# Kernel tuning notes

Measured on AMD Instinct MI355X. Metric: run time of the kernel, lower is better.

## Reference

```python
import jax, jax.numpy as jnp
import numpy as np

B, IN, K, T = 2048, 512, 16, 96
H = K // 2            # LSTM hidden per direction
L = IN - K + 1        # number of sliding patches


def setup_inputs() -> dict:
    key = jax.random.key(0)
    ks = jax.random.split(key, 16)
    def n(k, shape, s=0.1):
        return jax.random.normal(k, shape, dtype=jnp.float32) * s
    return {
        "x": jax.random.normal(ks[0], (B, IN), dtype=jnp.float32),
        "pe": n(ks[1], (L, K)),                                   # learnable positional encoding
        "W_seg": n(ks[2], (K, K)), "b_seg": jnp.zeros((K,), jnp.float32),
        "g_bn": jnp.ones((L,), jnp.float32), "b_bn": jnp.zeros((L,), jnp.float32),
        "Wih_f0": n(ks[3], (4 * H, K)),  "Whh_f0": n(ks[4], (4 * H, H)),
        "Wih_b0": n(ks[5], (4 * H, K)),  "Whh_b0": n(ks[6], (4 * H, H)),
        "Wih_f1": n(ks[7], (4 * H, 2 * H)), "Whh_f1": n(ks[8], (4 * H, H)),
        "Wih_b1": n(ks[9], (4 * H, 2 * H)), "Whh_b1": n(ks[10], (4 * H, H)),
        "g_ln": jnp.ones((K,), jnp.float32), "b_ln": jnp.zeros((K,), jnp.float32),
        "W1": n(ks[11], (512, K)), "b1": jnp.zeros((512,), jnp.float32),
        "W2": n(ks[12], (1, 512)), "b2": jnp.zeros((1,), jnp.float32),
    }


def _cell(h, c, x_t, Wih, Whh):
    # PyTorch LSTM cell, no bias; gate order i,f,g,o
    g = x_t @ Wih.T + h @ Whh.T
    i, f, gg, o = jnp.split(g, 4, axis=-1)
    c_new = jax.nn.sigmoid(f) * c + jax.nn.sigmoid(i) * jnp.tanh(gg)
    h_new = jax.nn.sigmoid(o) * jnp.tanh(c_new)
    return h_new, c_new


def _run_dir(xs, Wih, Whh, reverse):
    # xs: [B, L, D]; one LSTM direction via lax.scan over time
    z = jnp.zeros((xs.shape[0], Whh.shape[1]), xs.dtype)
    def step(carry, x_t):
        h, c = carry
        h, c = _cell(h, c, x_t, Wih, Whh)
        return (h, c), h
    (hT, cT), ys = jax.lax.scan(step, (z, z), jnp.swapaxes(xs, 0, 1), reverse=reverse)
    return jnp.swapaxes(ys, 0, 1), hT, cT


def _ln(z, g, b, eps=1e-5):
    m = z.mean(-1, keepdims=True)
    v = ((z - m) ** 2).mean(-1, keepdims=True)
    return (z - m) * jax.lax.rsqrt(v + eps) * g + b


def reference(x, pe, W_seg, b_seg, g_bn, b_bn, Wih_f0, Whh_f0, Wih_b0, Whh_b0,
              Wih_f1, Whh_f1, Wih_b1, Whh_b1, g_ln, b_ln, W1, b1, W2, b2):
    # SegmentationBlock: unfold -> +PE -> Linear -> GELU -> BatchNorm1d(L)
    idx = jnp.arange(L)[:, None] + jnp.arange(K)[None, :]
    p = x[:, idx] + pe                                     # [B, L, K]
    p = jax.nn.gelu(p @ W_seg.T + b_seg, approximate=False)
    mu = p.mean(axis=(0, 2), keepdims=True)                # BN over channel dim L (batch stats)
    var = p.var(axis=(0, 2), keepdims=True)
    xe = (p - mu) * jax.lax.rsqrt(var + 1e-5) * g_bn[None, :, None] + b_bn[None, :, None]
    # 2-layer bidirectional LSTM encoder
    of0, hf0, cf0 = _run_dir(xe, Wih_f0, Whh_f0, False)
    ob0, hb0, cb0 = _run_dir(xe, Wih_b0, Whh_b0, True)
    o0 = jnp.concatenate([of0, ob0], -1)                   # [B, L, 2H=K]
    of1, hf1, cf1 = _run_dir(o0, Wih_f1, Whh_f1, False)
    ob1, hb1, cb1 = _run_dir(o0, Wih_b1, Whh_b1, True)
    out = jnp.concatenate([of1, ob1], -1)                  # [B, L, K]
    out = _ln(out, g_ln, b_ln) + xe
    def dec(z):  # FCBlock, dropout off (eval)
        h = jax.nn.gelu(z @ W1.T + b1, approximate=False)
        return h @ W2.T + b2                               # [B, 1]
    fb = out[:, -1, :]                                     # [B, K]
    def step(carry, _):
        hf0, cf0, hb0, cb0, hf1, cf1, hb1, cb1, fb = carry
        hf0, cf0 = _cell(hf0, cf0, fb, Wih_f0, Whh_f0)
        hb0, cb0 = _cell(hb0, cb0, fb, Wih_b0, Whh_b0)
        m0 = jnp.concatenate([hf0, hb0], -1)
        hf1, cf1 = _cell(hf1, cf1, m0, Wih_f1, Whh_f1)
        hb1, cb1 = _cell(hb1, cb1, m0, Wih_b1, Whh_b1)
        o = jnp.concatenate([hf1, hb1], -1)                # [B, K]
        y = dec(_ln(o, g_ln, b_ln))[:, 0]                  # [B]
        return (hf0, cf0, hb0, cb0, hf1, cf1, hb1, cb1, o), y
    init = (hf0, cf0, hb0, cb0, hf1, cf1, hb1, cb1, fb)
    _, ys = jax.lax.scan(step, init, None, length=T)
    return jnp.swapaxes(ys, 0, 1)                          # [B, T]
```

## Files before the change

kernel.cpp:

```cpp
#include <hip/hip_runtime.h>
#include <math.h>

#define NB 2048
#define NIN 512
#define NK 16
#define NL 497
#define NT 96
#define NREP 32

__device__ __forceinline__ float gelu_exact(float x) {
    return 0.5f * x * (1.0f + erff(x * 0.70710678118654752440f));
}
__device__ __forceinline__ float gate_act(float acc, bool isG) {
    float mm = isG ? 2.0f : 1.0f;
    float e  = __expf(-mm * acc);
    float s  = 1.0f / (1.0f + e);
    return isG ? 2.0f * s - 1.0f : s;
}
__device__ __forceinline__ float tanh_safe(float x) {
    float t = __expf(-2.0f * fabsf(x));
    float r = 1.0f - 2.0f * t / (1.0f + t);
    return copysignf(r, x);
}
__device__ __forceinline__ void load16(const float* __restrict__ ptr, float* dst) {
    const float4* rp = (const float4*)ptr;
    float4 a = rp[0], b = rp[1], c = rp[2], d = rp[3];
    dst[0]=a.x; dst[1]=a.y; dst[2]=a.z;  dst[3]=a.w;
    dst[4]=b.x; dst[5]=b.y; dst[6]=b.z;  dst[7]=b.w;
    dst[8]=c.x; dst[9]=c.y; dst[10]=c.z; dst[11]=c.w;
    dst[12]=d.x;dst[13]=d.y;dst[14]=d.z; dst[15]=d.w;
}

template<int PRAW>
__global__ __launch_bounds__(256) void k_seg(
    const float* __restrict__ x, const float* __restrict__ pe,
    const float* __restrict__ Wseg, const float* __restrict__ bseg,
    const float* __restrict__ Wf0, const float* __restrict__ Wb0,
    float* __restrict__ praw, float* __restrict__ pfull,
    float* __restrict__ p_last, float* __restrict__ bn)
{
    __shared__ float xs[NIN];
    __shared__ float wsg[NK * NK];
    __shared__ float bs[NK];
    __shared__ float wf[32 * 16];
    __shared__ float wb[32 * 16];
    const int tid = threadIdx.x;
    const int b = blockIdx.x;
    float* bnr = bn + (size_t)(b & (NREP - 1)) * 1024;
    for (int i = tid; i < NIN; i += 256) xs[i] = x[(size_t)b * NIN + i];
    if (tid < NK * NK) wsg[tid] = Wseg[tid];
    if (tid < NK) bs[tid] = bseg[tid];
    if constexpr (PRAW) {
        for (int i = tid; i < 512; i += 256) { wf[i] = Wf0[i]; wb[i] = Wb0[i]; }
    }
    __syncthreads();

    for (int l = tid; l < NL; l += 256) {
        float u[NK];
        load16(pe + l * NK, u);
        #pragma unroll
        for (int k = 0; k < NK; k++) u[k] += xs[l + k];
        float p16[NK];
        float s = 0.f, s2 = 0.f;
        #pragma unroll
        for (int k = 0; k < NK; k++) {
            float acc = bs[k];
            #pragma unroll
            for (int kp = 0; kp < NK; kp++) acc += u[kp] * wsg[k * NK + kp];
            float gv = gelu_exact(acc);
            p16[k] = gv; s += gv; s2 += gv * gv;
        }
        atomicAdd(&bnr[l], s);
        atomicAdd(&bnr[512 + l], s2);

        if constexpr (PRAW) {
            float* pf = praw + ((size_t)b * NL + l) * 64;
            float* pb = praw + ((size_t)b * NL + (NL - 1 - l)) * 64 + 32;
            #pragma unroll 2
            for (int gq = 0; gq < 8; gq++) {
                float4 o;
                float* op = (float*)&o;
                #pragma unroll
                for (int q = 0; q < 4; q++) {
                    const float* wr = &wf[(gq * 4 + q) * 16];
                    float a0 = 0.f;
                    #pragma unroll
                    for (int k = 0; k < 16; k++) a0 += p16[k] * wr[k];
                    op[q] = a0;
                }
                ((float4*)pf)[gq] = o;
            }
            #pragma unroll 2
            for (int gq = 0; gq < 8; gq++) {
                float4 o;
                float* op = (float*)&o;
                #pragma unroll
                for (int q = 0; q < 4; q++) {
                    const float* wr = &wb[(gq * 4 + q) * 16];
                    float a0 = 0.f;
                    #pragma unroll
                    for (int k = 0; k < 16; k++) a0 += p16[k] * wr[k];
                    op[q] = a0;
                }
                ((float4*)pb)[gq] = o;
            }
        } else {
            float4* pr = (float4*)(pfull + ((size_t)b * NL + l) * NK);
            pr[0] = make_float4(p16[0], p16[1], p16[2], p16[3]);
            pr[1] = make_float4(p16[4], p16[5], p16[6], p16[7]);
            pr[2] = make_float4(p16[8], p16[9], p16[10], p16[11]);
            pr[3] = make_float4(p16[12], p16[13], p16[14], p16[15]);
        }
        if (l == NL - 1) {
            float4* pl = (float4*)(p_last + (size_t)b * NK);
            pl[0] = make_float4(p16[0], p16[1], p16[2], p16[3]);
            pl[1] = make_float4(p16[4], p16[5], p16[6], p16[7]);
            pl[2] = make_float4(p16[8], p16[9], p16[10], p16[11]);
            pl[3] = make_float4(p16[12], p16[13], p16[14], p16[15]);
        }
    }
}

__global__ void k_bnfin(const float* __restrict__ bn, const float* __restrict__ gbn,
                        const float* __restrict__ bbn, float* __restrict__ ansh4)
{
    int l = blockIdx.x * blockDim.x + threadIdx.x;
    if (l < NL) {
        float s = 0.f, s2 = 0.f;
        #pragma unroll 4
        for (int r = 0; r < NREP; r++) {
            s  += bn[(size_t)r * 1024 + l];
            s2 += bn[(size_t)r * 1024 + 512 + l];
        }
        const float inv = 1.0f / (float)(NB * NK);
        float mu  = s * inv;
        float var = s2 * inv - mu * mu;
        float rr  = rsqrtf(var + 1e-5f);
        float av  = gbn[l] * rr;
        float sh  = bbn[l] - mu * av;
        ansh4[4 * l]     = av;
        ansh4[4 * l + 1] = sh;
        int lr = NL - 1 - l;
        ansh4[4 * lr + 2] = av;
        ansh4[4 * lr + 3] = sh;
    }
}

template<int MODE, int WRITE_O, int WRITE_LAST>
__global__ __launch_bounds__(256) void k_lstm(
    const float* __restrict__ src, const float* __restrict__ ansh4,
    const float* __restrict__ WihF, const float* __restrict__ WhhF,
    const float* __restrict__ WihB, const float* __restrict__ WhhB,
    float* __restrict__ oout, float* __restrict__ st, float* __restrict__ oblast)
{
    const int tid = threadIdx.x;
    const int lane = tid & 63;
    const int b = blockIdx.x * 4 + (tid >> 6);
    const int d = lane >> 5, g = lane & 31, j = g & 7;
    const int base = d << 5;
    const float* Wih = d ? WihB : WihF;
    const float* Whh = d ? WhhB : WhhF;

    float whh[8];
    #pragma unroll
    for (int k = 0; k < 8; k++) whh[k] = Whh[g * 8 + k];

    float wih[16];
    float Sg = 0.f;
    if constexpr (MODE != 0) {
        #pragma unroll
        for (int k = 0; k < 16; k++) wih[k] = Wih[g * 16 + k];
        #pragma unroll
        for (int k = 0; k < 16; k++) Sg += wih[k];
    } else {
        #pragma unroll
        for (int k = 0; k < 16; k++) Sg += Wih[g * 16 + k];
    }

    float h = 0.f, c = 0.f;
    const bool isG = (g >= 16) && (g < 24);

    auto cell = [&](float acc, int s) {
        #pragma unroll
        for (int k = 0; k < 8; k++) acc += whh[k] * __shfl(h, base + k, 64);
        float val = gate_act(acc, isG);
        float fv = __shfl(val, lane + 8, 64);
        float gv = __shfl(val, lane + 16, 64);
        float ov = __shfl(val, lane + 24, 64);
        float cn = fv * c + val * gv;
        float hn = ov * tanh_safe(cn);
        if (g < 8) { c = cn; h = hn; }
        if constexpr (WRITE_O) {
            const int t = d ? (NL - 1 - s) : s;
            if (g < 8) oout[((size_t)b * NL + t) * NK + (d << 3) + j] = hn;
        }
        if constexpr (WRITE_LAST) {
            if (s == 0 && d == 1 && g < 8) oblast[b * 8 + j] = hn;
        }
    };

    if constexpr (MODE == 0) {
        const float* pr = src + (size_t)b * NL * 64 + lane;
        const float2* pa = (const float2*)ansh4 + d;
        float P0, P1, P2, P3;
        float2 A0, A1, A2, A3;
        P0 = pr[0];   A0 = pa[0];
        P1 = pr[64];  A1 = pa[2];
        P2 = pr[128]; A2 = pa[4];
        pr += 192; pa += 6;
        int s = 0;
        for (; s + 4 <= NL; s += 4) {
            P3 = pr[0];   A3 = pa[0]; cell(A0.x * P0 + A0.y * Sg, s);
            P0 = pr[64];  A0 = pa[2]; cell(A1.x * P1 + A1.y * Sg, s + 1);
            P1 = pr[128]; A1 = pa[4]; cell(A2.x * P2 + A2.y * Sg, s + 2);
            P2 = pr[192]; A2 = pa[6]; cell(A3.x * P3 + A3.y * Sg, s + 3);
            pr += 256; pa += 8;
        }
        if (s     < NL) cell(A0.x * P0 + A0.y * Sg, s);
        if (s + 1 < NL) cell(A1.x * P1 + A1.y * Sg, s + 1);
        if (s + 2 < NL) cell(A2.x * P2 + A2.y * Sg, s + 2);
    } else {
        const float* srcb = src + (size_t)b * NL * NK;
        auto rowt = [&](int sp) -> int {
            int t = d ? (NL - 1 - sp) : sp;
            t = t < 0 ? 0 : t;
            t = t > NL - 1 ? NL - 1 : t;
            return t;
        };
        auto ld = [&](int sp, float* dst, float2& a) {
            const int t = rowt(sp);
            load16(srcb + (size_t)t * NK, dst);
            if constexpr (MODE == 1) {
                int sc = sp > NL - 1 ? NL - 1 : sp;
                a = ((const float2*)ansh4)[2 * sc + d];
            }
        };
        auto stp = [&](int s, const float* B, float2 a) {
            float acc = 0.f;
            #pragma unroll
            for (int k = 0; k < 16; k++) acc += B[k] * wih[k];
            if constexpr (MODE == 1) acc = a.x * acc + a.y * Sg;
            cell(acc, s);
        };
        float B0[16], B1[16], B2[16], B3[16];
        float2 A0{0,0}, A1{0,0}, A2{0,0}, A3{0,0};
        ld(0, B0, A0); ld(1, B1, A1); ld(2, B2, A2);
        int s = 0;
        for (; s + 4 <= NL; s += 4) {
            ld(s + 3, B3, A3); stp(s + 0, B0, A0);
            ld(s + 4, B0, A0); stp(s + 1, B1, A1);
            ld(s + 5, B1, A1); stp(s + 2, B2, A2);
            ld(s + 6, B2, A2); stp(s + 3, B3, A3);
        }
        if (s     < NL) stp(s,     B0, A0);
        if (s + 1 < NL) stp(s + 1, B1, A1);
        if (s + 2 < NL) stp(s + 2, B2, A2);
    }

    if (g < 8) {
        float* hs = st + (d ? (size_t)2 * NB * 8 : 0);
        hs[b * 8 + j] = h;
        hs[(size_t)NB * 8 + b * 8 + j] = c;
    }
}

__global__ __launch_bounds__(256) void k_dec(
    const float* __restrict__ Wf0, const float* __restrict__ Uf0,
    const float* __restrict__ Wb0, const float* __restrict__ Ub0,
    const float* __restrict__ Wf1, const float* __restrict__ Uf1,
    const float* __restrict__ Wb1, const float* __restrict__ Ub1,
    const float* __restrict__ st0, const float* __restrict__ st1,
    const float* __restrict__ oblast, const float* __restrict__ p_last,
    const float* __restrict__ ansh4,
    const float* __restrict__ gln, const float* __restrict__ bln,
    float* __restrict__ z)
{
    const int tid = threadIdx.x, lane = tid & 63;
    const int b = blockIdx.x * 4 + (tid >> 6);
    const int d = lane >> 5, g = lane & 31, j = g & 7, base = d << 5;
    const float* Wih0 = d ? Wb0 : Wf0; const float* Whh0 = d ? Ub0 : Uf0;
    const float* Wih1 = d ? Wb1 : Wf1; const float* Whh1 = d ? Ub1 : Uf1;
    float wih0[16], whh0[8], wih1[16], whh1[8];
    #pragma unroll
    for (int k = 0; k < 16; k++) { wih0[k] = Wih0[g * 16 + k]; wih1[k] = Wih1[g * 16 + k]; }
    #pragma unroll
    for (int k = 0; k < 8; k++)  { whh0[k] = Whh0[g * 8 + k]; whh1[k] = Whh1[g * 8 + k]; }

    float h0 = 0.f, c0 = 0.f, h1 = 0.f, c1 = 0.f;
    if (g < 8) {
        const float* s0 = st0 + (d ? (size_t)2 * NB * 8 : 0);
        h0 = s0[b * 8 + j]; c0 = s0[(size_t)NB * 8 + b * 8 + j];
        const float* s1 = st1 + (d ? (size_t)2 * NB * 8 : 0);
        h1 = s1[b * 8 + j]; c1 = s1[(size_t)NB * 8 + b * 8 + j];
    }

    float fb[16];
    {
        float ol[16];
        #pragma unroll
        for (int k = 0; k < 8; k++) ol[k] = st1[b * 8 + k];
        #pragma unroll
        for (int k = 0; k < 8; k++) ol[8 + k] = oblast[b * 8 + k];
        float mn = 0.f;
        #pragma unroll
        for (int k = 0; k < 16; k++) mn += ol[k];
        mn *= (1.0f / 16.0f);
        float vv = 0.f;
        #pragma unroll
        for (int k = 0; k < 16; k++) { float dq = ol[k] - mn; vv += dq * dq; }
        vv *= (1.0f / 16.0f);
        float rr = rsqrtf(vv + 1e-5f);
        float aL = ansh4[4 * (NL - 1)], sL = ansh4[4 * (NL - 1) + 1];
        const float* prow = p_last + (size_t)b * NK;
        #pragma unroll
        for (int k = 0; k < 16; k++)
            fb[k] = (ol[k] - mn) * rr * gln[k] + bln[k] + (prow[k] * aL + sL);
    }

    const bool isG = (g >= 16) && (g < 24);
    for (int t = 0; t < NT; t++) {
        float acc = 0.f;
        #pragma unroll
        for (int k = 0; k < 16; k++) acc += fb[k] * wih0[k];
        #pragma unroll
        for (int k = 0; k < 8; k++) acc += whh0[k] * __shfl(h0, base + k, 64);
        float val = gate_act(acc, isG);
        float fv = __shfl(val, lane + 8, 64);
        float gv = __shfl(val, lane + 16, 64);
        float ov = __shfl(val, lane + 24, 64);
        float cn = fv * c0 + val * gv;
        float hn = ov * tanh_safe(cn);
        if (g < 8) { c0 = cn; h0 = hn; }
        float m0[16];
        #pragma unroll
        for (int k = 0; k < 16; k++) m0[k] = __shfl(h0, k < 8 ? k : 24 + k, 64);
        acc = 0.f;
        #pragma unroll
        for (int k = 0; k < 16; k++) acc += m0[k] * wih1[k];
        #pragma unroll
        for (int k = 0; k < 8; k++) acc += whh1[k] * __shfl(h1, base + k, 64);
        val = gate_act(acc, isG);
        fv = __shfl(val, lane + 8, 64);
        gv = __shfl(val, lane + 16, 64);
        ov = __shfl(val, lane + 24, 64);
        cn = fv * c1 + val * gv;
        hn = ov * tanh_safe(cn);
        if (g < 8) { c1 = cn; h1 = hn; }
        if (g < 8) z[((size_t)b * NT + t) * NK + (d << 3) + j] = hn;
        #pragma unroll
        for (int k = 0; k < 16; k++) fb[k] = __shfl(h1, k < 8 ? k : 24 + k, 64);
    }
}

__global__ __launch_bounds__(256) void k_head(
    const float* __restrict__ z, const float* __restrict__ gln, const float* __restrict__ bln,
    const float* __restrict__ W1, const float* __restrict__ b1,
    const float* __restrict__ W2, const float* __restrict__ b2,
    float* __restrict__ outp)
{
    __shared__ float w1s[512 * 16];
    __shared__ float b1s[512];
    __shared__ float w2s[512];
    const int tid = threadIdx.x;
    for (int i = tid; i < 512 * 16 / 4; i += 256)
        ((float4*)w1s)[i] = ((const float4*)W1)[i];
    for (int i = tid; i < 512; i += 256) { b1s[i] = b1[i]; w2s[i] = W2[i]; }
    __syncthreads();

    const size_t r = (size_t)blockIdx.x * 256 + tid;
    float zr[16];
    load16(z + r * 16, zr);
    float mn = 0.f;
    #pragma unroll
    for (int k = 0; k < 16; k++) mn += zr[k];
    mn *= (1.0f / 16.0f);
    float vv = 0.f;
    #pragma unroll
    for (int k = 0; k < 16; k++) { float dq = zr[k] - mn; vv += dq * dq; }
    vv *= (1.0f / 16.0f);
    float rr = rsqrtf(vv + 1e-5f);
    float zn[16];
    #pragma unroll
    for (int k = 0; k < 16; k++) zn[k] = (zr[k] - mn) * rr * gln[k] + bln[k];

    float y = b2[0];
    #pragma unroll 2
    for (int i = 0; i < 512; i++) {
        const float4* w4 = (const float4*)&w1s[i * 16];
        float4 wa = w4[0], wb = w4[1], wc = w4[2], wd = w4[3];
        float acc = b1s[i];
        acc += zn[0]*wa.x + zn[1]*wa.y + zn[2]*wa.z + zn[3]*wa.w;
        acc += zn[4]*wb.x + zn[5]*wb.y + zn[6]*wb.z + zn[7]*wb.w;
        acc += zn[8]*wc.x + zn[9]*wc.y + zn[10]*wc.z + zn[11]*wc.w;
        acc += zn[12]*wd.x + zn[13]*wd.y + zn[14]*wd.z + zn[15]*wd.w;
        y += gelu_exact(acc) * w2s[i];
    }
    outp[r] = y;
}

extern "C" void kernel_launch(void* const* d_in, const int* in_sizes, int n_in,
                              void* d_out, int out_size, void* d_ws, size_t ws_size,
                              hipStream_t stream)
{
    const float* x    = (const float*)d_in[0];
    const float* pe   = (const float*)d_in[1];
    const float* Wseg = (const float*)d_in[2];
    const float* bseg = (const float*)d_in[3];
    const float* gbn  = (const float*)d_in[4];
    const float* bbn  = (const float*)d_in[5];
    const float* Wf0  = (const float*)d_in[6];
    const float* Uf0  = (const float*)d_in[7];
    const float* Wb0  = (const float*)d_in[8];
    const float* Ub0  = (const float*)d_in[9];
    const float* Wf1  = (const float*)d_in[10];
    const float* Uf1  = (const float*)d_in[11];
    const float* Wb1  = (const float*)d_in[12];
    const float* Ub1  = (const float*)d_in[13];
    const float* gln  = (const float*)d_in[14];
    const float* bln  = (const float*)d_in[15];
    const float* W1   = (const float*)d_in[16];
    const float* b1   = (const float*)d_in[17];
    const float* W2   = (const float*)d_in[18];
    const float* b2   = (const float*)d_in[19];

    const size_t SZ_BN    = (size_t)NREP * 1024 * 4;
    const size_t SZ_ANSH  = (size_t)4 * 512 * 4;
    const size_t SZ_ST    = (size_t)4 * NB * 8 * 4;
    const size_t SZ_OBL   = (size_t)NB * 8 * 4;
    const size_t SZ_PLAST = (size_t)NB * NK * 4;
    const size_t SZ_Z     = (size_t)NB * NT * NK * 4;
    const size_t SZ_O0    = (size_t)NB * NL * NK * 4;
    const size_t SZ_PRAW  = (size_t)NB * NL * 64 * 4;
    const size_t GUARD    = 8192;

    char* ws = (char*)d_ws;
    size_t off = 0;
    auto take = [&](size_t bytes) -> char* {
        char* r = ws + off;
        off = (off + bytes + 255) & ~(size_t)255;
        return r;
    };
    float* bn     = (float*)take(SZ_BN);
    float* ansh4  = (float*)take(SZ_ANSH);
    float* st0    = (float*)take(SZ_ST);
    float* st1    = (float*)take(SZ_ST);
    float* obl    = (float*)take(SZ_OBL);
    float* p_last = (float*)take(SZ_PLAST);
    float* z      = (float*)take(SZ_Z);

    const size_t fixed = off;
    const size_t need_slim = fixed + SZ_O0 + SZ_PRAW + GUARD + 2048;
    const bool slim = (ws_size >= need_slim);

    hipMemsetAsync(bn, 0, SZ_BN, stream);

    if (slim) {
        float* o0   = (float*)take(SZ_O0);
        float* praw = (float*)take(SZ_PRAW);
        (void)take(GUARD);
        k_seg<1><<<NB, 256, 0, stream>>>(x, pe, Wseg, bseg, Wf0, Wb0, praw, nullptr, p_last, bn);
        k_bnfin<<<2, 256, 0, stream>>>(bn, gbn, bbn, ansh4);
        k_lstm<0, 1, 0><<<NB / 4, 256, 0, stream>>>(praw, ansh4, Wf0, Uf0, Wb0, Ub0, o0, st0, nullptr);
        k_lstm<2, 0, 1><<<NB / 4, 256, 0, stream>>>(o0, ansh4, Wf1, Uf1, Wb1, Ub1, nullptr, st1, obl);
    } else {
        float* p  = (float*)take(SZ_O0);
        float* o0 = (float*)take(SZ_O0);
        (void)take(GUARD);
        k_seg<0><<<NB, 256, 0, stream>>>(x, pe, Wseg, bseg, Wf0, Wb0, nullptr, p, p_last, bn);
        k_bnfin<<<2, 256, 0, stream>>>(bn, gbn, bbn, ansh4);
        k_lstm<1, 1, 0><<<NB / 4, 256, 0, stream>>>(p, ansh4, Wf0, Uf0, Wb0, Ub0, o0, st0, nullptr);
        k_lstm<2, 0, 1><<<NB / 4, 256, 0, stream>>>(o0, ansh4, Wf1, Uf1, Wb1, Ub1, nullptr, st1, obl);
    }
    k_dec<<<NB / 4, 256, 0, stream>>>(Wf0, Uf0, Wb0, Ub0, Wf1, Uf1, Wb1, Ub1,
                                      st0, st1, obl, p_last, ansh4, gln, bln, z);
    k_head<<<(NB * NT) / 256, 256, 0, stream>>>(z, gln, bln, W1, b1, W2, b2, (float*)d_out);
}
```

Measured before the change: 734.2 us.

## Remap LSTM to one hidden unit per lane over 8 batches, drop precomputed projections

The LSTM kernel now assigns each wave one direction and 8 batch rows, with each lane computing all four gates for one hidden unit. The recurrent state is exchanged via xor shuffles. The segmentation kernel no longer precomputes the 64-wide input projections into a large buffer; it writes the 16-wide patches and the LSTM does the input projection itself. This cuts large memory traffic and idle lanes, at the cost of far fewer waves for latency hiding and more serial work per step.

```diff
diff --git a/kernel.cpp b/kernel.cpp
--- a/kernel.cpp
+++ b/kernel.cpp
@@ -31,28 +31,20 @@
     dst[12]=d.x;dst[13]=d.y;dst[14]=d.z; dst[15]=d.w;
 }
 
-template<int PRAW>
 __global__ __launch_bounds__(256) void k_seg(
     const float* __restrict__ x, const float* __restrict__ pe,
     const float* __restrict__ Wseg, const float* __restrict__ bseg,
-    const float* __restrict__ Wf0, const float* __restrict__ Wb0,
-    float* __restrict__ praw, float* __restrict__ pfull,
-    float* __restrict__ p_last, float* __restrict__ bn)
+    float* __restrict__ p, float* __restrict__ p_last, float* __restrict__ bn)
 {
     __shared__ float xs[NIN];
     __shared__ float wsg[NK * NK];
     __shared__ float bs[NK];
-    __shared__ float wf[32 * 16];
-    __shared__ float wb[32 * 16];
     const int tid = threadIdx.x;
     const int b = blockIdx.x;
     float* bnr = bn + (size_t)(b & (NREP - 1)) * 1024;
     for (int i = tid; i < NIN; i += 256) xs[i] = x[(size_t)b * NIN + i];
     if (tid < NK * NK) wsg[tid] = Wseg[tid];
     if (tid < NK) bs[tid] = bseg[tid];
-    if constexpr (PRAW) {
-        for (int i = tid; i < 512; i += 256) { wf[i] = Wf0[i]; wb[i] = Wb0[i]; }
-    }
     __syncthreads();
 
     for (int l = tid; l < NL; l += 256) {
@@ -70,53 +62,16 @@
             float gv = gelu_exact(acc);
             p16[k] = gv; s += gv; s2 += gv * gv;
         }
+        float4* pr = (float4*)(p + ((size_t)b * NL + l) * NK);
+        pr[0] = make_float4(p16[0], p16[1], p16[2], p16[3]);
+        pr[1] = make_float4(p16[4], p16[5], p16[6], p16[7]);
+        pr[2] = make_float4(p16[8], p16[9], p16[10], p16[11]);
+        pr[3] = make_float4(p16[12], p16[13], p16[14], p16[15]);
         atomicAdd(&bnr[l], s);
         atomicAdd(&bnr[512 + l], s2);
-
-        if constexpr (PRAW) {
-            float* pf = praw + ((size_t)b * NL + l) * 64;
-            float* pb = praw + ((size_t)b * NL + (NL - 1 - l)) * 64 + 32;
-            #pragma unroll 2
-            for (int gq = 0; gq < 8; gq++) {
-                float4 o;
-                float* op = (float*)&o;
-                #pragma unroll
-                for (int q = 0; q < 4; q++) {
-                    const float* wr = &wf[(gq * 4 + q) * 16];
-                    float a0 = 0.f;
-                    #pragma unroll
-                    for (int k = 0; k < 16; k++) a0 += p16[k] * wr[k];
-                    op[q] = a0;
-                }
-                ((float4*)pf)[gq] = o;
-            }
-            #pragma unroll 2
-            for (int gq = 0; gq < 8; gq++) {
-                float4 o;
-                float* op = (float*)&o;
-                #pragma unroll
-                for (int q = 0; q < 4; q++) {
-                    const float* wr = &wb[(gq * 4 + q) * 16];
-                    float a0 = 0.f;
-                    #pragma unroll
-                    for (int k = 0; k < 16; k++) a0 += p16[k] * wr[k];
-                    op[q] = a0;
-                }
-                ((float4*)pb)[gq] = o;
-            }
-        } else {
-            float4* pr = (float4*)(pfull + ((size_t)b * NL + l) * NK);
-            pr[0] = make_float4(p16[0], p16[1], p16[2], p16[3]);
-            pr[1] = make_float4(p16[4], p16[5], p16[6], p16[7]);
-            pr[2] = make_float4(p16[8], p16[9], p16[10], p16[11]);
-            pr[3] = make_float4(p16[12], p16[13], p16[14], p16[15]);
-        }
         if (l == NL - 1) {
             float4* pl = (float4*)(p_last + (size_t)b * NK);
-            pl[0] = make_float4(p16[0], p16[1], p16[2], p16[3]);
-            pl[1] = make_float4(p16[4], p16[5], p16[6], p16[7]);
-            pl[2] = make_float4(p16[8], p16[9], p16[10], p16[11]);
-            pl[3] = make_float4(p16[12], p16[13], p16[14], p16[15]);
+            pl[0] = pr[0]; pl[1] = pr[1]; pl[2] = pr[2]; pl[3] = pr[3];
         }
     }
 }
@@ -147,121 +102,121 @@
 }
 
 template<int MODE, int WRITE_O, int WRITE_LAST>
-__global__ __launch_bounds__(256) void k_lstm(
+__global__ __launch_bounds__(256) void k_lstm8(
     const float* __restrict__ src, const float* __restrict__ ansh4,
     const float* __restrict__ WihF, const float* __restrict__ WhhF,
     const float* __restrict__ WihB, const float* __restrict__ WhhB,
     float* __restrict__ oout, float* __restrict__ st, float* __restrict__ oblast)
 {
     const int tid = threadIdx.x;
+    const int waveid = blockIdx.x * 4 + (tid >> 6);
     const int lane = tid & 63;
-    const int b = blockIdx.x * 4 + (tid >> 6);
-    const int d = lane >> 5, g = lane & 31, j = g & 7;
-    const int base = d << 5;
+    const int d = waveid & 1;
+    const int tile = waveid >> 1;
+    const int bh = lane >> 3;
+    const int u  = lane & 7;
+    const int b  = tile * 8 + bh;
+
     const float* Wih = d ? WihB : WihF;
     const float* Whh = d ? WhhB : WhhF;
 
-    float whh[8];
-    #pragma unroll
-    for (int k = 0; k < 8; k++) whh[k] = Whh[g * 8 + k];
-
-    float wih[16];
-    float Sg = 0.f;
-    if constexpr (MODE != 0) {
-        #pragma unroll
-        for (int k = 0; k < 16; k++) wih[k] = Wih[g * 16 + k];
-        #pragma unroll
-        for (int k = 0; k < 16; k++) Sg += wih[k];
-    } else {
-        #pragma unroll
-        for (int k = 0; k < 16; k++) Sg += Wih[g * 16 + k];
-    }
-
-    float h = 0.f, c = 0.f;
-    const bool isG = (g >= 16) && (g < 24);
-
-    auto cell = [&](float acc, int s) {
-        #pragma unroll
-        for (int k = 0; k < 8; k++) acc += whh[k] * __shfl(h, base + k, 64);
-        float val = gate_act(acc, isG);
-        float fv = __shfl(val, lane + 8, 64);
-        float gv = __shfl(val, lane + 16, 64);
-        float ov = __shfl(val, lane + 24, 64);
-        float cn = fv * c + val * gv;
-        float hn = ov * tanh_safe(cn);
-        if (g < 8) { c = cn; h = hn; }
-        if constexpr (WRITE_O) {
-            const int t = d ? (NL - 1 - s) : s;
-            if (g < 8) oout[((size_t)b * NL + t) * NK + (d << 3) + j] = hn;
-        }
+    float wih4[4][16], whh4[4][8], Sg4[4];
+    #pragma unroll
+    for (int gq = 0; gq < 4; gq++) {
+        const int row = (gq << 3) + u;
+        #pragma unroll
+        for (int k = 0; k < 16; k++) wih4[gq][k] = Wih[row * 16 + k];
+        #pragma unroll
+        for (int m = 0; m < 8; m++)  whh4[gq][m] = Whh[row * 8 + (u ^ m)];
+        float sg = 0.f;
+        if constexpr (MODE == 1) {
+            #pragma unroll
+            for (int k = 0; k < 16; k++) sg += wih4[gq][k];
+        }
+        Sg4[gq] = sg;
+    }
+
+    float c = 0.f;
+    float hx[8];
+    #pragma unroll
+    for (int m = 0; m < 8; m++) hx[m] = 0.f;
+
+    const int t0 = d ? NL - 1 : 0;
+    float* po = nullptr;
+    const int dstore = d ? -NK : NK;
+    if constexpr (WRITE_O) po = oout + ((size_t)b * NL + t0) * NK + (d << 3) + u;
+
+    auto stp = [&](int s, const float* B, float2 a) {
+        float d0 = 0.f, d1 = 0.f, d2 = 0.f, d3 = 0.f;
+        #pragma unroll
+        for (int k = 0; k < 16; k++) {
+            d0 += B[k] * wih4[0][k]; d1 += B[k] * wih4[1][k];
+            d2 += B[k] * wih4[2][k]; d3 += B[k] * wih4[3][k];
+        }
+        if constexpr (MODE == 1) {
+            d0 = a.x * d0 + a.y * Sg4[0]; d1 = a.x * d1 + a.y * Sg4[1];
+            d2 = a.x * d2 + a.y * Sg4[2]; d3 = a.x * d3 + a.y * Sg4[3];
+        }
+        #pragma unroll
+        for (int m = 0; m < 8; m++) {
+            d0 += whh4[0][m] * hx[m]; d1 += whh4[1][m] * hx[m];
+            d2 += whh4[2][m] * hx[m]; d3 += whh4[3][m] * hx[m];
+        }
+        float si = gate_act(d0, false);
+        float sf = gate_act(d1, false);
+        float tg = gate_act(d2, true);
+        float so = gate_act(d3, false);
+        float cn = sf * c + si * tg;
+        float hn = so * tanh_safe(cn);
+        c = cn;
+        float n0 = hn;
+        float n1 = __shfl_xor(n0, 1, 64);
+        float n2 = __shfl_xor(n0, 2, 64);
+        float n3 = __shfl_xor(n1, 2, 64);
+        float n4 = __shfl_xor(n0, 4, 64);
+        float n5 = __shfl_xor(n1, 4, 64);
+        float n6 = __shfl_xor(n2, 4, 64);
+        float n7 = __shfl_xor(n3, 4, 64);
+        hx[0] = n0; hx[1] = n1; hx[2] = n2; hx[3] = n3;
+        hx[4] = n4; hx[5] = n5; hx[6] = n6; hx[7] = n7;
+        if constexpr (WRITE_O) { *po = hn; po += dstore; }
         if constexpr (WRITE_LAST) {
-            if (s == 0 && d == 1 && g < 8) oblast[b * 8 + j] = hn;
+            if (s == 0 && d == 1) oblast[b * 8 + u] = hn;
         }
     };
 
-    if constexpr (MODE == 0) {
-        const float* pr = src + (size_t)b * NL * 64 + lane;
-        const float2* pa = (const float2*)ansh4 + d;
-        float P0, P1, P2, P3;
-        float2 A0, A1, A2, A3;
-        P0 = pr[0];   A0 = pa[0];
-        P1 = pr[64];  A1 = pa[2];
-        P2 = pr[128]; A2 = pa[4];
-        pr += 192; pa += 6;
-        int s = 0;
-        for (; s + 4 <= NL; s += 4) {
-            P3 = pr[0];   A3 = pa[0]; cell(A0.x * P0 + A0.y * Sg, s);
-            P0 = pr[64];  A0 = pa[2]; cell(A1.x * P1 + A1.y * Sg, s + 1);
-            P1 = pr[128]; A1 = pa[4]; cell(A2.x * P2 + A2.y * Sg, s + 2);
-            P2 = pr[192]; A2 = pa[6]; cell(A3.x * P3 + A3.y * Sg, s + 3);
-            pr += 256; pa += 8;
-        }
-        if (s     < NL) cell(A0.x * P0 + A0.y * Sg, s);
-        if (s + 1 < NL) cell(A1.x * P1 + A1.y * Sg, s + 1);
-        if (s + 2 < NL) cell(A2.x * P2 + A2.y * Sg, s + 2);
-    } else {
-        const float* srcb = src + (size_t)b * NL * NK;
-        auto rowt = [&](int sp) -> int {
-            int t = d ? (NL - 1 - sp) : sp;
-            t = t < 0 ? 0 : t;
-            t = t > NL - 1 ? NL - 1 : t;
-            return t;
-        };
-        auto ld = [&](int sp, float* dst, float2& a) {
-            const int t = rowt(sp);
-            load16(srcb + (size_t)t * NK, dst);
-            if constexpr (MODE == 1) {
-                int sc = sp > NL - 1 ? NL - 1 : sp;
-                a = ((const float2*)ansh4)[2 * sc + d];
-            }
-        };
-        auto stp = [&](int s, const float* B, float2 a) {
-            float acc = 0.f;
-            #pragma unroll
-            for (int k = 0; k < 16; k++) acc += B[k] * wih[k];
-            if constexpr (MODE == 1) acc = a.x * acc + a.y * Sg;
-            cell(acc, s);
-        };
-        float B0[16], B1[16], B2[16], B3[16];
-        float2 A0{0,0}, A1{0,0}, A2{0,0}, A3{0,0};
-        ld(0, B0, A0); ld(1, B1, A1); ld(2, B2, A2);
-        int s = 0;
-        for (; s + 4 <= NL; s += 4) {
-            ld(s + 3, B3, A3); stp(s + 0, B0, A0);
-            ld(s + 4, B0, A0); stp(s + 1, B1, A1);
-            ld(s + 5, B1, A1); stp(s + 2, B2, A2);
-            ld(s + 6, B2, A2); stp(s + 3, B3, A3);
-        }
-        if (s     < NL) stp(s,     B0, A0);
-        if (s + 1 < NL) stp(s + 1, B1, A1);
-        if (s + 2 < NL) stp(s + 2, B2, A2);
-    }
-
-    if (g < 8) {
-        float* hs = st + (d ? (size_t)2 * NB * 8 : 0);
-        hs[b * 8 + j] = h;
-        hs[(size_t)NB * 8 + b * 8 + j] = c;
-    }
+    const float* srcb = src + (size_t)b * NL * NK;
+    auto rowt = [&](int sp) -> int {
+        int t = d ? (NL - 1 - sp) : sp;
+        t = t < 0 ? 0 : t;
+        t = t > NL - 1 ? NL - 1 : t;
+        return t;
+    };
+    auto ld = [&](int sp, float* dst, float2& a) {
+        const int t = rowt(sp);
+        load16(srcb + (size_t)t * NK, dst);
+        if constexpr (MODE == 1) {
+            int sc = sp > NL - 1 ? NL - 1 : sp;
+            a = ((const float2*)ansh4)[2 * sc + d];
+        }
+    };
+    float B0[16], B1[16], B2[16], B3[16];
+    float2 A0{0,0}, A1{0,0}, A2{0,0}, A3{0,0};
+    ld(0, B0, A0); ld(1, B1, A1); ld(2, B2, A2);
+    int s = 0;
+    for (; s + 4 <= NL; s += 4) {
+        ld(s + 3, B3, A3); stp(s + 0, B0, A0);
+        ld(s + 4, B0, A0); stp(s + 1, B1, A1);
+        ld(s + 5, B1, A1); stp(s + 2, B2, A2);
+        ld(s + 6, B2, A2); stp(s + 3, B3, A3);
+    }
+    if (s     < NL) stp(s,     B0, A0);
+    if (s + 1 < NL) stp(s + 1, B1, A1);
+    if (s + 2 < NL) stp(s + 2, B2, A2);
+
+    float* hs = st + (d ? (size_t)2 * NB * 8 : 0);
+    hs[b * 8 + u] = hx[0];
+    hs[(size_t)NB * 8 + b * 8 + u] = c;
 }
 
 __global__ __launch_bounds__(256) void k_dec(
@@ -429,9 +384,7 @@
     const size_t SZ_OBL   = (size_t)NB * 8 * 4;
     const size_t SZ_PLAST = (size_t)NB * NK * 4;
     const size_t SZ_Z     = (size_t)NB * NT * NK * 4;
-    const size_t SZ_O0    = (size_t)NB * NL * NK * 4;
-    const size_t SZ_PRAW  = (size_t)NB * NL * 64 * 4;
-    const size_t GUARD    = 8192;
+    const size_t SZ_P     = (size_t)NB * NL * NK * 4;
 
     char* ws = (char*)d_ws;
     size_t off = 0;
@@ -447,30 +400,14 @@
     float* obl    = (float*)take(SZ_OBL);
     float* p_last = (float*)take(SZ_PLAST);
     float* z      = (float*)take(SZ_Z);
-
-    const size_t fixed = off;
-    const size_t need_slim = fixed + SZ_O0 + SZ_PRAW + GUARD + 2048;
-    const bool slim = (ws_size >= need_slim);
+    float* p      = (float*)take(SZ_P);
+    float* o0     = (float*)take(SZ_P);
 
     hipMemsetAsync(bn, 0, SZ_BN, stream);
-
-    if (slim) {
-        float* o0   = (float*)take(SZ_O0);
-        float* praw = (float*)take(SZ_PRAW);
-        (void)take(GUARD);
-        k_seg<1><<<NB, 256, 0, stream>>>(x, pe, Wseg, bseg, Wf0, Wb0, praw, nullptr, p_last, bn);
-        k_bnfin<<<2, 256, 0, stream>>>(bn, gbn, bbn, ansh4);
-        k_lstm<0, 1, 0><<<NB / 4, 256, 0, stream>>>(praw, ansh4, Wf0, Uf0, Wb0, Ub0, o0, st0, nullptr);
-        k_lstm<2, 0, 1><<<NB / 4, 256, 0, stream>>>(o0, ansh4, Wf1, Uf1, Wb1, Ub1, nullptr, st1, obl);
-    } else {
-        float* p  = (float*)take(SZ_O0);
-        float* o0 = (float*)take(SZ_O0);
-        (void)take(GUARD);
-        k_seg<0><<<NB, 256, 0, stream>>>(x, pe, Wseg, bseg, Wf0, Wb0, nullptr, p, p_last, bn);
-        k_bnfin<<<2, 256, 0, stream>>>(bn, gbn, bbn, ansh4);
-        k_lstm<1, 1, 0><<<NB / 4, 256, 0, stream>>>(p, ansh4, Wf0, Uf0, Wb0, Ub0, o0, st0, nullptr);
-        k_lstm<2, 0, 1><<<NB / 4, 256, 0, stream>>>(o0, ansh4, Wf1, Uf1, Wb1, Ub1, nullptr, st1, obl);
-    }
+    k_seg<<<NB, 256, 0, stream>>>(x, pe, Wseg, bseg, p, p_last, bn);
+    k_bnfin<<<2, 256, 0, stream>>>(bn, gbn, bbn, ansh4);
+    k_lstm8<1, 1, 0><<<128, 256, 0, stream>>>(p, ansh4, Wf0, Uf0, Wb0, Ub0, o0, st0, nullptr);
+    k_lstm8<2, 0, 1><<<128, 256, 0, stream>>>(o0, ansh4, Wf1, Uf1, Wb1, Ub1, nullptr, st1, obl);
     k_dec<<<NB / 4, 256, 0, stream>>>(Wf0, Uf0, Wb0, Ub0, Wf1, Uf1, Wb1, Ub1,
                                       st0, st1, obl, p_last, ansh4, gln, bln, z);
     k_head<<<(NB * NT) / 256, 256, 0, stream>>>(z, gln, bln, W1, b1, W2, b2, (float*)d_out);
```

After: 859.0 us. 17.0% more time.

## Remap LSTM to 8 lanes per sequence with bpermute and precomputed layer-1 projections

Applied to the files above, without the earlier changes.

Replaces the layer LSTM kernels with a new mapping. Each lane now owns one hidden unit and computes all four gates, so 8 sequences share a wave and each wave handles one direction. Hidden-state exchange uses ds_bpermute with XOR-permuted weights, which removes the per-gate cross-lane shuffles. A new projection kernel precomputes the layer-1 input projections for both directions into a gate-interleaved buffer, and the praw layout is reordered to match. The cost is an extra kernel pass and extra global traffic for layer 1, plus more registers per lane.

```diff
diff --git a/kernel.cpp b/kernel.cpp
--- a/kernel.cpp
+++ b/kernel.cpp
@@ -21,6 +21,9 @@
     float t = __expf(-2.0f * fabsf(x));
     float r = 1.0f - 2.0f * t / (1.0f + t);
     return copysignf(r, x);
+}
+__device__ __forceinline__ float bperm(int idxb, float v) {
+    return __int_as_float(__builtin_amdgcn_ds_bpermute(idxb, __float_as_int(v)));
 }
 __device__ __forceinline__ void load16(const float* __restrict__ ptr, float* dst) {
     const float4* rp = (const float4*)ptr;
@@ -74,35 +77,23 @@
         atomicAdd(&bnr[512 + l], s2);
 
         if constexpr (PRAW) {
-            float* pf = praw + ((size_t)b * NL + l) * 64;
-            float* pb = praw + ((size_t)b * NL + (NL - 1 - l)) * 64 + 32;
+            float4* pf = (float4*)(praw + (((size_t)b * NL + l) * 2 + 0) * 32);
+            float4* pb = (float4*)(praw + (((size_t)b * NL + (NL - 1 - l)) * 2 + 1) * 32);
             #pragma unroll 2
-            for (int gq = 0; gq < 8; gq++) {
-                float4 o;
-                float* op = (float*)&o;
+            for (int uu = 0; uu < 8; uu++) {
+                float4 of, ob;
+                float* ofp = (float*)&of;
+                float* obp = (float*)&ob;
                 #pragma unroll
-                for (int q = 0; q < 4; q++) {
-                    const float* wr = &wf[(gq * 4 + q) * 16];
-                    float a0 = 0.f;
+                for (int gq = 0; gq < 4; gq++) {
+                    const float* wrf = &wf[(gq * 8 + uu) * 16];
+                    const float* wrb = &wb[(gq * 8 + uu) * 16];
+                    float a0 = 0.f, a1 = 0.f;
                     #pragma unroll
-                    for (int k = 0; k < 16; k++) a0 += p16[k] * wr[k];
-                    op[q] = a0;
+                    for (int k = 0; k < 16; k++) { a0 += p16[k] * wrf[k]; a1 += p16[k] * wrb[k]; }
+                    ofp[gq] = a0; obp[gq] = a1;
                 }
-                ((float4*)pf)[gq] = o;
-            }
-            #pragma unroll 2
-            for (int gq = 0; gq < 8; gq++) {
-                float4 o;
-                float* op = (float*)&o;
-                #pragma unroll
-                for (int q = 0; q < 4; q++) {
-                    const float* wr = &wb[(gq * 4 + q) * 16];
-                    float a0 = 0.f;
-                    #pragma unroll
-                    for (int k = 0; k < 16; k++) a0 += p16[k] * wr[k];
-                    op[q] = a0;
-                }
-                ((float4*)pb)[gq] = o;
+                pf[uu] = of; pb[uu] = ob;
             }
         } else {
             float4* pr = (float4*)(pfull + ((size_t)b * NL + l) * NK);
@@ -146,8 +137,148 @@
     }
 }
 
+__global__ __launch_bounds__(256) void k_proj(
+    const float* __restrict__ o0, const float* __restrict__ Wf1,
+    const float* __restrict__ Wb1, float* __restrict__ praw)
+{
+    __shared__ float wf[512], wb[512];
+    const int tid = threadIdx.x;
+    const int b = blockIdx.x;
+    for (int i = tid; i < 512; i += 256) { wf[i] = Wf1[i]; wb[i] = Wb1[i]; }
+    __syncthreads();
+    for (int l = tid; l < NL; l += 256) {
+        float v[16];
+        load16(o0 + ((size_t)b * NL + l) * NK, v);
+        float4* pf = (float4*)(praw + (((size_t)b * NL + l) * 2 + 0) * 32);
+        float4* pb = (float4*)(praw + (((size_t)b * NL + (NL - 1 - l)) * 2 + 1) * 32);
+        #pragma unroll 2
+        for (int uu = 0; uu < 8; uu++) {
+            float4 of, ob;
+            float* ofp = (float*)&of;
+            float* obp = (float*)&ob;
+            #pragma unroll
+            for (int gq = 0; gq < 4; gq++) {
+                const float* wrf = &wf[(gq * 8 + uu) * 16];
+                const float* wrb = &wb[(gq * 8 + uu) * 16];
+                float a0 = 0.f, a1 = 0.f;
+                #pragma unroll
+                for (int k = 0; k < 16; k++) { a0 += v[k] * wrf[k]; a1 += v[k] * wrb[k]; }
+                ofp[gq] = a0; obp[gq] = a1;
+            }
+            pf[uu] = of; pb[uu] = ob;
+        }
+    }
+}
+
 template<int MODE, int WRITE_O, int WRITE_LAST>
-__global__ __launch_bounds__(256) void k_lstm(
+__global__ __launch_bounds__(64) void k_lstm8p(
+    const float* __restrict__ praw, const float* __restrict__ ansh4,
+    const float* __restrict__ WihF, const float* __restrict__ WihB,
+    const float* __restrict__ WhhF, const float* __restrict__ WhhB,
+    float* __restrict__ oout, float* __restrict__ st, float* __restrict__ oblast)
+{
+    const int waveid = blockIdx.x;
+    const int lane = threadIdx.x;
+    const int d = waveid & 1;
+    const int tile = waveid >> 1;
+    const int bh = lane >> 3, u = lane & 7;
+    const int b = tile * 8 + bh;
+
+    const float* Whh = d ? WhhB : WhhF;
+    float whh4[4][8];
+    #pragma unroll
+    for (int gq = 0; gq < 4; gq++) {
+        const int row = (gq << 3) + u;
+        #pragma unroll
+        for (int m = 0; m < 8; m++) whh4[gq][m] = Whh[row * 8 + (u ^ m)];
+    }
+    float Sg4[4] = {0.f, 0.f, 0.f, 0.f};
+    if constexpr (MODE == 1) {
+        const float* Wih = d ? WihB : WihF;
+        #pragma unroll
+        for (int gq = 0; gq < 4; gq++) {
+            const int row = (gq << 3) + u;
+            float sg = 0.f;
+            #pragma unroll
+            for (int k = 0; k < 16; k++) sg += Wih[row * 16 + k];
+            Sg4[gq] = sg;
+        }
+    }
+    int bidx[8];
+    #pragma unroll
+    for (int m = 0; m < 8; m++) bidx[m] = ((lane & 56) | (u ^ m)) << 2;
+
+    float c = 0.f;
+    float hx[8];
+    #pragma unroll
+    for (int m = 0; m < 8; m++) hx[m] = 0.f;
+
+    float* po = nullptr;
+    const int dst = d ? -NK : NK;
+    if constexpr (WRITE_O) po = oout + ((size_t)b * NL + (d ? NL - 1 : 0)) * NK + (d << 3) + u;
+
+    auto cell = [&](float4 P, float2 a, int s) {
+        float a0, a1, a2, a3;
+        if constexpr (MODE == 1) {
+            a0 = a.x * P.x + a.y * Sg4[0];
+            a1 = a.x * P.y + a.y * Sg4[1];
+            a2 = a.x * P.z + a.y * Sg4[2];
+            a3 = a.x * P.w + a.y * Sg4[3];
+        } else {
+            a0 = P.x; a1 = P.y; a2 = P.z; a3 = P.w;
+        }
+        #pragma unroll
+        for (int m = 0; m < 8; m++) {
+            a0 += whh4[0][m] * hx[m]; a1 += whh4[1][m] * hx[m];
+            a2 += whh4[2][m] * hx[m]; a3 += whh4[3][m] * hx[m];
+        }
+        float si = gate_act(a0, false);
+        float sf = gate_act(a1, false);
+        float tg = gate_act(a2, true);
+        float so = gate_act(a3, false);
+        float cn = sf * c + si * tg;
+        float hn = so * tanh_safe(cn);
+        c = cn;
+        hx[0] = hn;
+        hx[1] = bperm(bidx[1], hn);
+        hx[2] = bperm(bidx[2], hn);
+        hx[3] = bperm(bidx[3], hn);
+        hx[4] = bperm(bidx[4], hn);
+        hx[5] = bperm(bidx[5], hn);
+        hx[6] = bperm(bidx[6], hn);
+        hx[7] = bperm(bidx[7], hn);
+        if constexpr (WRITE_O) { *po = hn; po += dst; }
+        if constexpr (WRITE_LAST) {
+            if (s == 0 && d == 1) oblast[b * 8 + u] = hn;
+        }
+    };
+
+    const float4* pr = (const float4*)praw + (((size_t)b * NL * 2) + d) * 8 + u;
+    const float2* pa = (const float2*)ansh4 + d;
+    float4 P0, P1, P2, P3;
+    float2 A0{0,0}, A1{0,0}, A2{0,0}, A3{0,0};
+    P0 = pr[0];  P1 = pr[16]; P2 = pr[32];
+    if constexpr (MODE == 1) { A0 = pa[0]; A1 = pa[2]; A2 = pa[4]; }
+    pr += 48; pa += 6;
+    int s = 0;
+    for (; s + 4 <= NL; s += 4) {
+        P3 = pr[0];  if constexpr (MODE == 1) A3 = pa[0]; cell(P0, A0, s);
+        P0 = pr[16]; if constexpr (MODE == 1) A0 = pa[2]; cell(P1, A1, s + 1);
+        P1 = pr[32]; if constexpr (MODE == 1) A1 = pa[4]; cell(P2, A2, s + 2);
+        P2 = pr[48]; if constexpr (MODE == 1) A2 = pa[6]; cell(P3, A3, s + 3);
+        pr += 64; pa += 8;
+    }
+    if (s     < NL) cell(P0, A0, s);
+    if (s + 1 < NL) cell(P1, A1, s + 1);
+    if (s + 2 < NL) cell(P2, A2, s + 2);
+
+    float* hs = st + (d ? (size_t)2 * NB * 8 : 0);
+    hs[b * 8 + u] = hx[0];
+    hs[(size_t)NB * 8 + b * 8 + u] = c;
+}
+
+template<int MODE, int WRITE_O, int WRITE_LAST>
+__global__ __launch_bounds__(256) void k_lstmA(
     const float* __restrict__ src, const float* __restrict__ ansh4,
     const float* __restrict__ WihF, const float* __restrict__ WhhF,
     const float* __restrict__ WihB, const float* __restrict__ WhhB,
@@ -160,26 +291,19 @@
     const int base = d << 5;
     const float* Wih = d ? WihB : WihF;
     const float* Whh = d ? WhhB : WhhF;
-
     float whh[8];
     #pragma unroll
     for (int k = 0; k < 8; k++) whh[k] = Whh[g * 8 + k];
-
     float wih[16];
     float Sg = 0.f;
-    if constexpr (MODE != 0) {
-        #pragma unroll
-        for (int k = 0; k < 16; k++) wih[k] = Wih[g * 16 + k];
+    #pragma unroll
+    for (int k = 0; k < 16; k++) wih[k] = Wih[g * 16 + k];
+    if constexpr (MODE == 1) {
         #pragma unroll
         for (int k = 0; k < 16; k++) Sg += wih[k];
-    } else {
-        #pragma unroll
-        for (int k = 0; k < 16; k++) Sg += Wih[g * 16 + k];
-    }
-
+    }
     float h = 0.f, c = 0.f;
     const bool isG = (g >= 16) && (g < 24);
-
     auto cell = [&](float acc, int s) {
         #pragma unroll
         for (int k = 0; k < 8; k++) acc += whh[k] * __shfl(h, base + k, 64);
@@ -198,65 +322,41 @@
             if (s == 0 && d == 1 && g < 8) oblast[b * 8 + j] = hn;
         }
     };
-
-    if constexpr (MODE == 0) {
-        const float* pr = src + (size_t)b * NL * 64 + lane;
-        const float2* pa = (const float2*)ansh4 + d;
-        float P0, P1, P2, P3;
-        float2 A0, A1, A2, A3;
-        P0 = pr[0];   A0 = pa[0];
-        P1 = pr[64];  A1 = pa[2];
-        P2 = pr[128]; A2 = pa[4];
-        pr += 192; pa += 6;
-        int s = 0;
-        for (; s + 4 <= NL; s += 4) {
-            P3 = pr[0];   A3 = pa[0]; cell(A0.x * P0 + A0.y * Sg, s);
-            P0 = pr[64];  A0 = pa[2]; cell(A1.x * P1 + A1.y * Sg, s + 1);
-            P1 = pr[128]; A1 = pa[4]; cell(A2.x * P2 + A2.y * Sg, s + 2);
-            P2 = pr[192]; A2 = pa[6]; cell(A3.x * P3 + A3.y * Sg, s + 3);
-            pr += 256; pa += 8;
-        }
-        if (s     < NL) cell(A0.x * P0 + A0.y * Sg, s);
-        if (s + 1 < NL) cell(A1.x * P1 + A1.y * Sg, s + 1);
-        if (s + 2 < NL) cell(A2.x * P2 + A2.y * Sg, s + 2);
-    } else {
-        const float* srcb = src + (size_t)b * NL * NK;
-        auto rowt = [&](int sp) -> int {
-            int t = d ? (NL - 1 - sp) : sp;
-            t = t < 0 ? 0 : t;
-            t = t > NL - 1 ? NL - 1 : t;
-            return t;
-        };
-        auto ld = [&](int sp, float* dst, float2& a) {
-            const int t = rowt(sp);
-            load16(srcb + (size_t)t * NK, dst);
-            if constexpr (MODE == 1) {
-                int sc = sp > NL - 1 ? NL - 1 : sp;
-                a = ((const float2*)ansh4)[2 * sc + d];
-            }
-        };
-        auto stp = [&](int s, const float* B, float2 a) {
-            float acc = 0.f;
-            #pragma unroll
-            for (int k = 0; k < 16; k++) acc += B[k] * wih[k];
-            if constexpr (MODE == 1) acc = a.x * acc + a.y * Sg;
-            cell(acc, s);
-        };
-        float B0[16], B1[16], B2[16], B3[16];
-        float2 A0{0,0}, A1{0,0}, A2{0,0}, A3{0,0};
-        ld(0, B0, A0); ld(1, B1, A1); ld(2, B2, A2);
-        int s = 0;
-        for (; s + 4 <= NL; s += 4) {
-            ld(s + 3, B3, A3); stp(s + 0, B0, A0);
-            ld(s + 4, B0, A0); stp(s + 1, B1, A1);
-            ld(s + 5, B1, A1); stp(s + 2, B2, A2);
-            ld(s + 6, B2, A2); stp(s + 3, B3, A3);
-        }
-        if (s     < NL) stp(s,     B0, A0);
-        if (s + 1 < NL) stp(s + 1, B1, A1);
-        if (s + 2 < NL) stp(s + 2, B2, A2);
-    }
-
+    const float* srcb = src + (size_t)b * NL * NK;
+    auto rowt = [&](int sp) -> int {
+        int t = d ? (NL - 1 - sp) : sp;
+        t = t < 0 ? 0 : t;
+        t = t > NL - 1 ? NL - 1 : t;
+        return t;
+    };
+    auto ld = [&](int sp, float* dstv, float2& a) {
+        const int t = rowt(sp);
+        load16(srcb + (size_t)t * NK, dstv);
+        if constexpr (MODE == 1) {
+            int sc = sp > NL - 1 ? NL - 1 : sp;
+            a = ((const float2*)ansh4)[2 * sc + d];
+        }
+    };
+    auto stp = [&](int s, const float* B, float2 a) {
+        float acc = 0.f;
+        #pragma unroll
+        for (int k = 0; k < 16; k++) acc += B[k] * wih[k];
+        if constexpr (MODE == 1) acc = a.x * acc + a.y * Sg;
+        cell(acc, s);
+    };
+    float B0[16], B1[16], B2[16], B3[16];
+    float2 A0{0,0}, A1{0,0}, A2{0,0}, A3{0,0};
+    ld(0, B0, A0); ld(1, B1, A1); ld(2, B2, A2);
+    int s = 0;
+    for (; s + 4 <= NL; s += 4) {
+        ld(s + 3, B3, A3); stp(s + 0, B0, A0);
+        ld(s + 4, B0, A0); stp(s + 1, B1, A1);
+        ld(s + 5, B1, A1); stp(s + 2, B2, A2);
+        ld(s + 6, B2, A2); stp(s + 3, B3, A3);
+    }
+    if (s     < NL) stp(s,     B0, A0);
+    if (s + 1 < NL) stp(s + 1, B1, A1);
+    if (s + 2 < NL) stp(s + 2, B2, A2);
     if (g < 8) {
         float* hs = st + (d ? (size_t)2 * NB * 8 : 0);
         hs[b * 8 + j] = h;
@@ -429,7 +529,7 @@
     const size_t SZ_OBL   = (size_t)NB * 8 * 4;
     const size_t SZ_PLAST = (size_t)NB * NK * 4;
     const size_t SZ_Z     = (size_t)NB * NT * NK * 4;
-    const size_t SZ_O0    = (size_t)NB * NL * NK * 4;
+    const size_t SZ_P     = (size_t)NB * NL * NK * 4;
     const size_t SZ_PRAW  = (size_t)NB * NL * 64 * 4;
     const size_t GUARD    = 8192;
 
@@ -449,27 +549,28 @@
     float* z      = (float*)take(SZ_Z);
 
     const size_t fixed = off;
-    const size_t need_slim = fixed + SZ_O0 + SZ_PRAW + GUARD + 2048;
-    const bool slim = (ws_size >= need_slim);
+    const size_t need_praw = fixed + SZ_P + SZ_PRAW + GUARD + 2048;
+    const bool use_praw = (ws_size >= need_praw);
 
     hipMemsetAsync(bn, 0, SZ_BN, stream);
 
-    if (slim) {
-        float* o0   = (float*)take(SZ_O0);
+    if (use_praw) {
+        float* o0   = (float*)take(SZ_P);
         float* praw = (float*)take(SZ_PRAW);
         (void)take(GUARD);
         k_seg<1><<<NB, 256, 0, stream>>>(x, pe, Wseg, bseg, Wf0, Wb0, praw, nullptr, p_last, bn);
         k_bnfin<<<2, 256, 0, stream>>>(bn, gbn, bbn, ansh4);
-        k_lstm<0, 1, 0><<<NB / 4, 256, 0, stream>>>(praw, ansh4, Wf0, Uf0, Wb0, Ub0, o0, st0, nullptr);
-        k_lstm<2, 0, 1><<<NB / 4, 256, 0, stream>>>(o0, ansh4, Wf1, Uf1, Wb1, Ub1, nullptr, st1, obl);
+        k_lstm8p<1, 1, 0><<<512, 64, 0, stream>>>(praw, ansh4, Wf0, Wb0, Uf0, Ub0, o0, st0, nullptr);
+        k_proj<<<NB, 256, 0, stream>>>(o0, Wf1, Wb1, praw);
+        k_lstm8p<2, 0, 1><<<512, 64, 0, stream>>>(praw, nullptr, nullptr, nullptr, Uf1, Ub1, nullptr, st1, obl);
     } else {
-        float* p  = (float*)take(SZ_O0);
-        float* o0 = (float*)take(SZ_O0);
+        float* p  = (float*)take(SZ_P);
+        float* o0 = (float*)take(SZ_P);
         (void)take(GUARD);
         k_seg<0><<<NB, 256, 0, stream>>>(x, pe, Wseg, bseg, Wf0, Wb0, nullptr, p, p_last, bn);
         k_bnfin<<<2, 256, 0, stream>>>(bn, gbn, bbn, ansh4);
-        k_lstm<1, 1, 0><<<NB / 4, 256, 0, stream>>>(p, ansh4, Wf0, Uf0, Wb0, Ub0, o0, st0, nullptr);
-        k_lstm<2, 0, 1><<<NB / 4, 256, 0, stream>>>(o0, ansh4, Wf1, Uf1, Wb1, Ub1, nullptr, st1, obl);
+        k_lstmA<1, 1, 0><<<NB / 4, 256, 0, stream>>>(p, ansh4, Wf0, Uf0, Wb0, Ub0, o0, st0, nullptr);
+        k_lstmA<2, 0, 1><<<NB / 4, 256, 0, stream>>>(o0, ansh4, Wf1, Uf1, Wb1, Ub1, nullptr, st1, obl);
     }
     k_dec<<<NB / 4, 256, 0, stream>>>(Wf0, Uf0, Wb0, Ub0, Wf1, Uf1, Wb1, Ub1,
                                       st0, st1, obl, p_last, ansh4, gln, bln, z);
```

Measured after the change: 736.0 us. No clear change (+0.2%).
